# Kernel tuning notes

Hardware: AMD Instinct MI355X
Metric: run time of the kernel (lower is better)

## Reference

```python
import jax, jax.numpy as jnp
import numpy as np

EMBED_DIM = 1024
NUM_HEADS = 16
HEAD_DIM = EMBED_DIM // NUM_HEADS
BATCH = 8
SEQ = 1024


def setup_inputs() -> dict:
    key = jax.random.key(0)
    ks = jax.random.split(key, 10)
    s = 1.0 / np.sqrt(EMBED_DIM)
    x = jax.random.normal(ks[0], (BATCH, SEQ, EMBED_DIM), dtype=jnp.float32)
    mask = jax.random.randint(ks[1], (BATCH, SEQ), 0, 2, dtype=jnp.int32)
    mk = lambda k: (jax.random.normal(k, (EMBED_DIM, EMBED_DIM), dtype=jnp.float32) * s)
    return {
        "x": x, "mask": mask,
        "Wq": mk(ks[2]), "bq": jnp.zeros((EMBED_DIM,), jnp.float32),
        "Wk": mk(ks[3]), "bk": jnp.zeros((EMBED_DIM,), jnp.float32),
        "Wv": mk(ks[4]), "bv": jnp.zeros((EMBED_DIM,), jnp.float32),
        "Wo": mk(ks[5]), "bo": jnp.zeros((EMBED_DIM,), jnp.float32),
    }


def _split_heads(t):
    # (B, S, E) -> (B, H, S, D)
    B, S, _ = t.shape
    return t.reshape(B, S, NUM_HEADS, HEAD_DIM).transpose(0, 2, 1, 3)


def reference(x, mask, Wq, bq, Wk, bk, Wv, bv, Wo, bo):
    B, S, E = x.shape
    # torch Linear: y = x @ W.T + b, weight shape (out, in)
    Q = _split_heads(jnp.einsum('bse,oe->bso', x, Wq) + bq)
    K = _split_heads(jnp.einsum('bse,oe->bso', x, Wk) + bk)
    V = _split_heads(jnp.einsum('bse,oe->bso', x, Wv) + bv)
    scores = jnp.einsum('bhqd,bhkd->bhqk', Q, K) / np.sqrt(HEAD_DIM)
    scores = jnp.clip(scores, -50.0, 50.0)
    m = (mask == 0)[:, None, None, :]  # (B,1,1,S)
    scores = jnp.where(m, jnp.float32(-1e9), scores)
    scores = jnp.where(jnp.isfinite(scores), scores, jnp.zeros_like(scores))
    aw = jax.nn.softmax(scores, axis=-1)
    aw = jnp.where(jnp.isfinite(aw), aw, jnp.zeros_like(aw))
    aw = aw / (aw.sum(axis=-1, keepdims=True) + 1e-10)
    # dropout is identity in eval mode
    attended = jnp.einsum('bhqk,bhkd->bhqd', aw, V)
    attended = attended.transpose(0, 2, 1, 3).reshape(B, S, E)
    output = jnp.einsum('bse,oe->bso', attended, Wo) + bo
    return (output, aw)
```

## Files before the change

kernel.cpp:

```cpp
#include <hip/hip_runtime.h>
#include <stdint.h>

typedef _Float16 f16x8 __attribute__((ext_vector_type(8)));
typedef float    f32x4 __attribute__((ext_vector_type(4)));

#define SEQL 1024
#define EMB  1024
#define NH   16
#define HD   64
#define BATCH 8
#define QKVN 3072

__device__ __forceinline__ void gll16(const void* g, void* l) {
  __builtin_amdgcn_global_load_lds(
      (const __attribute__((address_space(1))) unsigned int*)(uintptr_t)g,
      (__attribute__((address_space(3))) unsigned int*)(uintptr_t)l, 16, 0, 0);
}

__device__ __forceinline__ void cvt8(const float* __restrict__ in,
                                     _Float16* __restrict__ out, int i) {
  const float4* p = (const float4*)in;
  float4 a = p[2 * i], b = p[2 * i + 1];
  f16x8 o;
  o[0] = (_Float16)a.x; o[1] = (_Float16)a.y; o[2] = (_Float16)a.z; o[3] = (_Float16)a.w;
  o[4] = (_Float16)b.x; o[5] = (_Float16)b.y; o[6] = (_Float16)b.z; o[7] = (_Float16)b.w;
  ((f16x8*)out)[i] = o;
}

__global__ __launch_bounds__(256) void k_prep(const float* __restrict__ x,
                                              const float* __restrict__ Wq,
                                              const float* __restrict__ Wk,
                                              const float* __restrict__ Wv,
                                              const float* __restrict__ Wo,
                                              const float* __restrict__ bq,
                                              const float* __restrict__ bk,
                                              const float* __restrict__ bv,
                                              _Float16* __restrict__ x16,
                                              _Float16* __restrict__ Wqkv16,
                                              _Float16* __restrict__ Wo16,
                                              float* __restrict__ bqkv) {
  const int bid = blockIdx.x, tid = threadIdx.x;
  if (bid < 4096) {
    cvt8(x, x16, bid * 256 + tid);
  } else if (bid < 4608) {
    cvt8(Wq, Wqkv16, (bid - 4096) * 256 + tid);
  } else if (bid < 5120) {
    cvt8(Wk, Wqkv16 + (size_t)EMB * EMB, (bid - 4608) * 256 + tid);
  } else if (bid < 5632) {
    cvt8(Wv, Wqkv16 + (size_t)2 * EMB * EMB, (bid - 5120) * 256 + tid);
  } else if (bid < 6144) {
    cvt8(Wo, Wo16, (bid - 5632) * 256 + tid);
  } else {
    int i = (bid - 6144) * 256 + tid;
    float v = (i < 1024) ? bq[i] : (i < 2048 ? bk[i - 1024] : bv[i - 2048]);
    bqkv[i] = v;
  }
}

template <int OUT_F16>
__global__ __launch_bounds__(256) void k_gemm_nt(const _Float16* __restrict__ A,
                                                 const _Float16* __restrict__ B,
                                                 const float* __restrict__ bias,
                                                 void* __restrict__ Cv,
                                                 int M, int N, int K) {
  __shared__ __align__(16) _Float16 As[128 * 32];
  __shared__ __align__(16) _Float16 Bs[128 * 32];
  const int nb = N >> 7;
  const int bm = (int)blockIdx.x / nb, bn = (int)blockIdx.x % nb;
  const int m0 = bm << 7, n0 = bn << 7;
  const int tid = threadIdx.x;
  const int wave = tid >> 6, lane = tid & 63, quad = lane >> 4, l16 = lane & 15;
  const int wm = (wave & 1) << 6, wn = (wave >> 1) << 6;

  f32x4 acc[4][4] = {};

  const int c0 = tid, c1 = tid + 256;
  const int row0 = c0 >> 2, ko0 = (c0 & 3) << 3;
  const int row1 = c1 >> 2, ko1 = (c1 & 3) << 3;
  const _Float16* a0 = A + (size_t)(m0 + row0) * K + ko0;
  const _Float16* a1 = A + (size_t)(m0 + row1) * K + ko1;
  const _Float16* b0 = B + (size_t)(n0 + row0) * K + ko0;
  const _Float16* b1 = B + (size_t)(n0 + row1) * K + ko1;

  for (int k0 = 0; k0 < K; k0 += 32) {
    __syncthreads();
    gll16(a0 + k0, As + (size_t)c0 * 8);
    gll16(a1 + k0, As + (size_t)c1 * 8);
    gll16(b0 + k0, Bs + (size_t)c0 * 8);
    gll16(b1 + k0, Bs + (size_t)c1 * 8);
    __syncthreads();

    f16x8 af[4], bf[4];
#pragma unroll
    for (int i = 0; i < 4; ++i)
      af[i] = *(const f16x8*)(As + ((wm + (i << 4) + l16) << 5) + (quad << 3));
#pragma unroll
    for (int i = 0; i < 4; ++i)
      bf[i] = *(const f16x8*)(Bs + ((wn + (i << 4) + l16) << 5) + (quad << 3));
#pragma unroll
    for (int i = 0; i < 4; ++i)
#pragma unroll
      for (int j = 0; j < 4; ++j)
        acc[i][j] = __builtin_amdgcn_mfma_f32_16x16x32_f16(af[i], bf[j], acc[i][j], 0, 0, 0);
  }

#pragma unroll
  for (int j = 0; j < 4; ++j) {
    int col = n0 + wn + (j << 4) + l16;
    float bb = bias[col];
#pragma unroll
    for (int i = 0; i < 4; ++i) {
      int rowb = m0 + wm + (i << 4) + (quad << 2);
#pragma unroll
      for (int r = 0; r < 4; ++r) {
        float v = acc[i][j][r] + bb;
        if (OUT_F16)
          ((_Float16*)Cv)[(size_t)(rowb + r) * N + col] = (_Float16)v;
        else
          ((float*)Cv)[(size_t)(rowb + r) * N + col] = v;
      }
    }
  }
}

__global__ __launch_bounds__(256) void k_transpose_v(const _Float16* __restrict__ QKV,
                                                     _Float16* __restrict__ Vt) {
  int tid = blockIdx.x * 256 + threadIdx.x;
  int d = tid & 63;
  int s0 = ((tid >> 6) & 127) << 3;
  int h = (tid >> 13) & 15;
  int b = tid >> 17;
  const _Float16* src = QKV + ((size_t)(b * SEQL + s0)) * QKVN + 2048 + h * HD + d;
  f16x8 t;
#pragma unroll
  for (int j = 0; j < 8; ++j) t[j] = src[(size_t)j * QKVN];
  *(f16x8*)(Vt + ((size_t)((b * NH + h) * HD + d)) * SEQL + s0) = t;
}

#define PPAD2 136
#define OPAD 68

__global__ __launch_bounds__(256, 4) void k_attn_fused(const _Float16* __restrict__ QKV,
                                                       const _Float16* __restrict__ Vt,
                                                       const int* __restrict__ mask,
                                                       float* __restrict__ aw,
                                                       _Float16* __restrict__ att) {
  __shared__ __align__(16) _Float16 kbuf[8192];
  __shared__ __align__(16) char pob[4][4352];
  __shared__ float sm[4][16], sl[4][16];

  const int qt = blockIdx.x, h = blockIdx.y, b = blockIdx.z;
  const int tid = threadIdx.x;
  const int wave = tid >> 6, lane = tid & 63, quad = lane >> 4, l16 = lane & 15;

  const _Float16* Qbase =
      QKV + ((size_t)(b * SEQL + qt * 16 + l16)) * QKVN + h * HD + quad * 8;
  f16x8 qf0 = *(const f16x8*)(Qbase);
  f16x8 qf1 = *(const f16x8*)(Qbase + 32);

  float p[16][4];
  float mr[4], lr[4];
#pragma unroll
  for (int r = 0; r < 4; ++r) mr[r] = -3.0e38f;

  const int* mrow = mask + b * SEQL;

  const _Float16* Kg = QKV + (size_t)b * SEQL * QKVN + 1024 + h * HD;
  const int krow = tid >> 3;
  const int kdch = (tid & 7) ^ (krow & 7);
  const _Float16* Kme = Kg + (size_t)krow * QKVN + kdch * 8;
  _Float16* kdst = kbuf + (size_t)tid * 8;

  for (int c = 0; c < 8; ++c) {
    if (c) __syncthreads();
#pragma unroll
    for (int g = 0; g < 4; ++g)
      gll16(Kme + (size_t)(c * 128 + g * 32) * QKVN, kdst + (size_t)g * 2048);
    __syncthreads();
#pragma unroll
    for (int ctw = 0; ctw < 2; ++ctw) {
      int sloc = wave * 32 + ctw * 16 + l16;
      int ch0 = sloc * 8 + (quad ^ (sloc & 7));
      f16x8 kf0 = *(const f16x8*)(kbuf + (size_t)ch0 * 8);
      f16x8 kf1 = *(const f16x8*)(kbuf + (size_t)(ch0 ^ 4) * 8);
      f32x4 acc = {};
      acc = __builtin_amdgcn_mfma_f32_16x16x32_f16(qf0, kf0, acc, 0, 0, 0);
      acc = __builtin_amdgcn_mfma_f32_16x16x32_f16(qf1, kf1, acc, 0, 0, 0);
      int col = c * 128 + sloc;
      bool mk = (mrow[col] == 0);
      int pidx = c * 2 + ctw;
#pragma unroll
      for (int r = 0; r < 4; ++r) {
        float s = acc[r] * 0.125f;
        s = fminf(fmaxf(s, -50.f), 50.f);
        if (mk) s = -1.0e9f;
        p[pidx][r] = s;
        mr[r] = fmaxf(mr[r], s);
      }
    }
  }

#pragma unroll
  for (int r = 0; r < 4; ++r) {
    float m = mr[r];
    m = fmaxf(m, __shfl_xor(m, 1, 16));
    m = fmaxf(m, __shfl_xor(m, 2, 16));
    m = fmaxf(m, __shfl_xor(m, 4, 16));
    m = fmaxf(m, __shfl_xor(m, 8, 16));
    mr[r] = m;
  }
#pragma unroll
  for (int r = 0; r < 4; ++r) lr[r] = 0.f;
#pragma unroll
  for (int pidx = 0; pidx < 16; ++pidx) {
#pragma unroll
    for (int r = 0; r < 4; ++r) {
      float e = __expf(p[pidx][r] - mr[r]);
      p[pidx][r] = e;
      lr[r] += e;
    }
  }
#pragma unroll
  for (int r = 0; r < 4; ++r) {
    float l = lr[r];
    l += __shfl_xor(l, 1, 16);
    l += __shfl_xor(l, 2, 16);
    l += __shfl_xor(l, 4, 16);
    l += __shfl_xor(l, 8, 16);
    lr[r] = l;
  }
  if (l16 == 0) {
#pragma unroll
    for (int r = 0; r < 4; ++r) {
      sm[wave][quad * 4 + r] = mr[r];
      sl[wave][quad * 4 + r] = lr[r];
    }
  }
  __syncthreads();

  float f[4];
#pragma unroll
  for (int r = 0; r < 4; ++r) {
    int row = quad * 4 + r;
    float M = fmaxf(fmaxf(sm[0][row], sm[1][row]), fmaxf(sm[2][row], sm[3][row]));
    float L = sl[0][row] * __expf(sm[0][row] - M) + sl[1][row] * __expf(sm[1][row] - M) +
              sl[2][row] * __expf(sm[2][row] - M) + sl[3][row] * __expf(sm[3][row] - M);
    f[r] = __expf(mr[r] - M) / L;
  }

  float* awb = aw + (((size_t)(b * NH + h)) * SEQL + qt * 16) * SEQL;
  _Float16* pw = (_Float16*)pob[wave];
  const _Float16* vtb = Vt + ((size_t)(b * NH + h)) * HD * SEQL;
  f32x4 opv[4] = {};
#pragma unroll
  for (int hf = 0; hf < 2; ++hf) {
#pragma unroll
    for (int pl = 0; pl < 8; ++pl) {
      int pidx = hf * 8 + pl;
      int col = ((pidx >> 1) << 7) + (wave << 5) + ((pidx & 1) << 4) + l16;
#pragma unroll
      for (int r = 0; r < 4; ++r) {
        float v = p[pidx][r] * f[r];
        awb[(size_t)(quad * 4 + r) * SEQL + col] = v;
        pw[(quad * 4 + r) * PPAD2 + pl * 16 + l16] = (_Float16)v;
      }
    }
#pragma unroll
    for (int j = 0; j < 4; ++j) {
      f16x8 af = *(const f16x8*)(pw + l16 * PPAD2 + j * 32 + quad * 8);
      int sbase = ((hf * 4 + j) << 7) + (wave << 5) + (quad << 3);
#pragma unroll
      for (int nt = 0; nt < 4; ++nt) {
        f16x8 bf = *(const f16x8*)(vtb + (size_t)(nt * 16 + l16) * SEQL + sbase);
        opv[nt] = __builtin_amdgcn_mfma_f32_16x16x32_f16(af, bf, opv[nt], 0, 0, 0);
      }
    }
  }

  float* ob = (float*)&pob[0][0];
#pragma unroll
  for (int nt = 0; nt < 4; ++nt)
#pragma unroll
    for (int r = 0; r < 4; ++r)
      ob[(wave * 16 + quad * 4 + r) * OPAD + nt * 16 + l16] = opv[nt][r];
  __syncthreads();

  {
    int col = tid & 63;
    int r0 = tid >> 6;
#pragma unroll
    for (int i = 0; i < 4; ++i) {
      int row = r0 + i * 4;
      float o = ob[row * OPAD + col] + ob[(16 + row) * OPAD + col] +
                ob[(32 + row) * OPAD + col] + ob[(48 + row) * OPAD + col];
      att[((size_t)(b * SEQL + qt * 16 + row)) * EMB + h * HD + col] = (_Float16)o;
    }
  }
}

extern "C" void kernel_launch(void* const* d_in, const int* in_sizes, int n_in,
                              void* d_out, int out_size, void* d_ws, size_t ws_size,
                              hipStream_t stream) {
  const float* x  = (const float*)d_in[0];
  const int* mask = (const int*)d_in[1];
  const float* Wq = (const float*)d_in[2];
  const float* bq = (const float*)d_in[3];
  const float* Wk = (const float*)d_in[4];
  const float* bk = (const float*)d_in[5];
  const float* Wv = (const float*)d_in[6];
  const float* bv = (const float*)d_in[7];
  const float* Wo = (const float*)d_in[8];
  const float* bo = (const float*)d_in[9];

  float* out = (float*)d_out;
  float* aw = out + (size_t)BATCH * SEQL * EMB;

  char* ws = (char*)d_ws;
  _Float16* x16    = (_Float16*)(ws);
  _Float16* Wqkv16 = (_Float16*)(ws + ((size_t)16 << 20));
  _Float16* Wo16   = (_Float16*)(ws + ((size_t)22 << 20));
  float*    bqkv   = (float*)   (ws + ((size_t)24 << 20));
  _Float16* QKV16  = (_Float16*)(ws + ((size_t)25 << 20));
  _Float16* Vt16   = (_Float16*)(ws + ((size_t)73 << 20));
  _Float16* att16  = (_Float16*)(ws + ((size_t)89 << 20));

  const int M = BATCH * SEQL;

  k_prep<<<6156, 256, 0, stream>>>(x, Wq, Wk, Wv, Wo, bq, bk, bv,
                                   x16, Wqkv16, Wo16, bqkv);

  k_gemm_nt<1><<<(M / 128) * (QKVN / 128), 256, 0, stream>>>(x16, Wqkv16, bqkv, QKV16,
                                                             M, QKVN, EMB);

  k_transpose_v<<<4096, 256, 0, stream>>>(QKV16, Vt16);

  k_attn_fused<<<dim3(SEQL / 16, NH, BATCH), 256, 0, stream>>>(QKV16, Vt16, mask, aw, att16);

  k_gemm_nt<0><<<(M / 128) * (EMB / 128), 256, 0, stream>>>(att16, Wo16, bo, out,
                                                            M, EMB, EMB);
}
```

Before: 912.7 us.

## Load K directly from global, swizzle grid for XCD locality, nontemporal aw stores

Drops the shared-memory staging of K and the eight barrier pairs in the attention kernel. Each wave now reads its own contiguous 256-key slice straight from global memory into MFMA operands, and the column mapping for P and V is remapped to match. The grid is flattened and swizzled so that consecutive blocks on the same XCD share a (b,h), which improves L2 reuse of K and V. The attention-weight output is written with nontemporal stores to avoid polluting the cache. The trade-off is that K is now read once per wave instead of once per block, through L2, using uncoalesced 16-byte row reads.

Result: faster. 868.4 us (-4.8%).

```diff
diff --git a/kernel.cpp b/kernel.cpp
--- a/kernel.cpp
+++ b/kernel.cpp
@@ -145,11 +145,13 @@
                                                        const int* __restrict__ mask,
                                                        float* __restrict__ aw,
                                                        _Float16* __restrict__ att) {
-  __shared__ __align__(16) _Float16 kbuf[8192];
   __shared__ __align__(16) char pob[4][4352];
   __shared__ float sm[4][16], sl[4][16];
 
-  const int qt = blockIdx.x, h = blockIdx.y, b = blockIdx.z;
+  const int wg = (int)blockIdx.x;
+  const int swz = ((wg & 7) << 10) | (wg >> 3);
+  const int qt = swz & 63, h = (swz >> 6) & 15, b = swz >> 10;
+
   const int tid = threadIdx.x;
   const int wave = tid >> 6, lane = tid & 63, quad = lane >> 4, l16 = lane & 15;
 
@@ -165,38 +167,24 @@
 
   const int* mrow = mask + b * SEQL;
 
-  const _Float16* Kg = QKV + (size_t)b * SEQL * QKVN + 1024 + h * HD;
-  const int krow = tid >> 3;
-  const int kdch = (tid & 7) ^ (krow & 7);
-  const _Float16* Kme = Kg + (size_t)krow * QKVN + kdch * 8;
-  _Float16* kdst = kbuf + (size_t)tid * 8;
-
-  for (int c = 0; c < 8; ++c) {
-    if (c) __syncthreads();
-#pragma unroll
-    for (int g = 0; g < 4; ++g)
-      gll16(Kme + (size_t)(c * 128 + g * 32) * QKVN, kdst + (size_t)g * 2048);
-    __syncthreads();
-#pragma unroll
-    for (int ctw = 0; ctw < 2; ++ctw) {
-      int sloc = wave * 32 + ctw * 16 + l16;
-      int ch0 = sloc * 8 + (quad ^ (sloc & 7));
-      f16x8 kf0 = *(const f16x8*)(kbuf + (size_t)ch0 * 8);
-      f16x8 kf1 = *(const f16x8*)(kbuf + (size_t)(ch0 ^ 4) * 8);
-      f32x4 acc = {};
-      acc = __builtin_amdgcn_mfma_f32_16x16x32_f16(qf0, kf0, acc, 0, 0, 0);
-      acc = __builtin_amdgcn_mfma_f32_16x16x32_f16(qf1, kf1, acc, 0, 0, 0);
-      int col = c * 128 + sloc;
-      bool mk = (mrow[col] == 0);
-      int pidx = c * 2 + ctw;
-#pragma unroll
-      for (int r = 0; r < 4; ++r) {
-        float s = acc[r] * 0.125f;
-        s = fminf(fmaxf(s, -50.f), 50.f);
-        if (mk) s = -1.0e9f;
-        p[pidx][r] = s;
-        mr[r] = fmaxf(mr[r], s);
-      }
+  const _Float16* Kb0 = QKV + (size_t)b * SEQL * QKVN + 1024 + h * HD + quad * 8;
+#pragma unroll
+  for (int ct = 0; ct < 16; ++ct) {
+    int col = (wave << 8) + (ct << 4) + l16;
+    const _Float16* Kb = Kb0 + (size_t)col * QKVN;
+    f16x8 kf0 = *(const f16x8*)(Kb);
+    f16x8 kf1 = *(const f16x8*)(Kb + 32);
+    f32x4 acc = {};
+    acc = __builtin_amdgcn_mfma_f32_16x16x32_f16(qf0, kf0, acc, 0, 0, 0);
+    acc = __builtin_amdgcn_mfma_f32_16x16x32_f16(qf1, kf1, acc, 0, 0, 0);
+    bool mk = (mrow[col] == 0);
+#pragma unroll
+    for (int r = 0; r < 4; ++r) {
+      float s = acc[r] * 0.125f;
+      s = fminf(fmaxf(s, -50.f), 50.f);
+      if (mk) s = -1.0e9f;
+      p[ct][r] = s;
+      mr[r] = fmaxf(mr[r], s);
     }
   }
 
@@ -257,18 +245,18 @@
 #pragma unroll
     for (int pl = 0; pl < 8; ++pl) {
       int pidx = hf * 8 + pl;
-      int col = ((pidx >> 1) << 7) + (wave << 5) + ((pidx & 1) << 4) + l16;
+      int col = (wave << 8) + (pidx << 4) + l16;
 #pragma unroll
       for (int r = 0; r < 4; ++r) {
         float v = p[pidx][r] * f[r];
-        awb[(size_t)(quad * 4 + r) * SEQL + col] = v;
+        __builtin_nontemporal_store(v, &awb[(size_t)(quad * 4 + r) * SEQL + col]);
         pw[(quad * 4 + r) * PPAD2 + pl * 16 + l16] = (_Float16)v;
       }
     }
 #pragma unroll
     for (int j = 0; j < 4; ++j) {
       f16x8 af = *(const f16x8*)(pw + l16 * PPAD2 + j * 32 + quad * 8);
-      int sbase = ((hf * 4 + j) << 7) + (wave << 5) + (quad << 3);
+      int sbase = (wave << 8) + (hf << 7) + (j << 5) + (quad << 3);
 #pragma unroll
       for (int nt = 0; nt < 4; ++nt) {
         f16x8 bf = *(const f16x8*)(vtb + (size_t)(nt * 16 + l16) * SEQL + sbase);
@@ -334,7 +322,7 @@
 
   k_transpose_v<<<4096, 256, 0, stream>>>(QKV16, Vt16);
 
-  k_attn_fused<<<dim3(SEQL / 16, NH, BATCH), 256, 0, stream>>>(QKV16, Vt16, mask, aw, att16);
+  k_attn_fused<<<SEQL / 16 * NH * BATCH, 256, 0, stream>>>(QKV16, Vt16, mask, aw, att16);
 
   k_gemm_nt<0><<<(M / 128) * (EMB / 128), 256, 0, stream>>>(att16, Wo16, bo, out,
                                                             M, EMB, EMB);
```
